# Optimization experiments

Hardware: AMD Instinct MI355X
Metric: run time of the kernel (lower is better)

Reference implementation:

```python
import jax, jax.numpy as jnp
import numpy as np

N_NODES = 100000
N_EDGES = 1600000
IN_DIM = 128
OUT_DIM = 10
N_GRAPHS = 512


def setup_inputs() -> dict:
    key = jax.random.key(0)
    ks = jax.random.split(key, 16)
    x = jax.random.normal(ks[0], (N_NODES, IN_DIM), dtype=jnp.float32)
    edge_index = jax.random.randint(ks[1], (2, N_EDGES), 0, N_NODES, dtype=jnp.int64)
    batch = jnp.sort(jax.random.randint(ks[2], (N_NODES,), 0, N_GRAPHS, dtype=jnp.int64))
    s = 0.1
    params = {
        'W1': jax.random.normal(ks[3], (IN_DIM, 32), dtype=jnp.float32) * s,
        'b1': jnp.zeros((32,), dtype=jnp.float32),
        'W2': jax.random.normal(ks[4], (32, 64), dtype=jnp.float32) * s,
        'b2': jnp.zeros((64,), dtype=jnp.float32),
        'W3': jax.random.normal(ks[5], (64, 128), dtype=jnp.float32) * s,
        'b3': jnp.zeros((128,), dtype=jnp.float32),
        'Wl1': jax.random.normal(ks[6], (128, 64), dtype=jnp.float32) * s,
        'bl1': jnp.zeros((64,), dtype=jnp.float32),
        'Wl2': jax.random.normal(ks[7], (64, OUT_DIM), dtype=jnp.float32) * s,
        'bl2': jnp.zeros((OUT_DIM,), dtype=jnp.float32),
    }
    return {'x': x, 'edge_index': edge_index, 'batch': batch, **params}


def _gcn_conv(x, src, dst, norm, W, b, n):
    # PyG GCNConv: out[i] = sum_j norm_ij * (x[j] @ W) + b, with self-loops folded into (src, dst).
    xw = x @ W                                   # [N, F_out]
    msg = xw[src] * norm[:, None]                # gather + scale  [E+N, F_out]
    return jax.ops.segment_sum(msg, dst, num_segments=n) + b


def reference(x, edge_index, batch, W1, b1, W2, b2, W3, b3, Wl1, bl1, Wl2, bl2):
    n = x.shape[0]
    loops = jnp.arange(n, dtype=edge_index.dtype)
    src = jnp.concatenate([edge_index[0], loops])  # j (source)
    dst = jnp.concatenate([edge_index[1], loops])  # i (target)
    # symmetric normalization D^{-1/2} (A+I) D^{-1/2}; degree at targets incl. self-loops
    deg = jax.ops.segment_sum(jnp.ones_like(dst, dtype=x.dtype), dst, num_segments=n)
    dinv = jnp.where(deg > 0, jax.lax.rsqrt(deg), 0.0)
    norm = dinv[src] * dinv[dst]
    # eval mode: dropout is identity
    h = jax.nn.relu(_gcn_conv(x, src, dst, norm, W1, b1, n))
    h = jax.nn.relu(_gcn_conv(h, src, dst, norm, W2, b2, n))
    h = _gcn_conv(h, src, dst, norm, W3, b3, n)
    g = jax.ops.segment_sum(h, batch, num_segments=N_GRAPHS)  # global_add_pool
    g = jax.nn.relu(g @ Wl1 + bl1)
    g = g @ Wl2 + bl2
    return jax.nn.log_softmax(g, axis=1)
```

## Files before the change

kernel.cpp:

```cpp
#include <hip/hip_runtime.h>
#include <hip/hip_bf16.h>
#include <math.h>
#include <type_traits>

#define NN 100000
#define NE 1600000
#define NG 512
#define NPB 128
#define NBUCK ((NN + NPB - 1) / NPB)
#define BCAP 3072
#define PBLOCKS 256
#define PTHREADS 1024

__device__ __forceinline__ float b2f(ushort u){ return __uint_as_float(((unsigned int)u)<<16); }
__device__ __forceinline__ ushort f2b(float f){
    __hip_bfloat16 h = __float2bfloat16(f);
    return *(ushort*)&h;
}
__device__ __forceinline__ float blo(unsigned int u){ return __uint_as_float(u<<16); }
__device__ __forceinline__ float bhi(unsigned int u){ return __uint_as_float(u & 0xffff0000u); }
__device__ __forceinline__ void acc4(float* a, uint2 u){
    a[0] += blo(u.x); a[1] += bhi(u.x); a[2] += blo(u.y); a[3] += bhi(u.y);
}
__device__ __forceinline__ void acc8(float* a, uint4 u){
    a[0] += blo(u.x); a[1] += bhi(u.x); a[2] += blo(u.y); a[3] += bhi(u.y);
    a[4] += blo(u.z); a[5] += bhi(u.z); a[6] += blo(u.w); a[7] += bhi(u.w);
}

__global__ __launch_bounds__(PTHREADS) void part_kernel(const int* __restrict__ src, const int* __restrict__ dst,
                                                        int* __restrict__ bucket_cnt, int* __restrict__ recs, int e){
    __shared__ int hist[NBUCK];
    __shared__ int base_[NBUCK];
    int tid = threadIdx.x;
    for(int b=tid; b<NBUCK; b+=PTHREADS) hist[b]=0;
    __syncthreads();
    int per = (e + PBLOCKS - 1) / PBLOCKS;
    per = (per + 3) & ~3;
    int lo = blockIdx.x * per;
    int hi = lo + per; if(hi > e) hi = e;
    if(lo >= hi) return;
    const int4* __restrict__ dst4 = (const int4*)dst;
    const int4* __restrict__ src4 = (const int4*)src;
    for(int i=lo/4+tid; i<hi/4; i+=PTHREADS){
        int4 d = dst4[i];
        atomicAdd(&hist[d.x>>7], 1);
        atomicAdd(&hist[d.y>>7], 1);
        atomicAdd(&hist[d.z>>7], 1);
        atomicAdd(&hist[d.w>>7], 1);
    }
    __syncthreads();
    for(int b=tid; b<NBUCK; b+=PTHREADS){
        int h = hist[b];
        base_[b] = h ? atomicAdd(&bucket_cnt[b], h) : 0;
        hist[b] = 0;
    }
    __syncthreads();
    for(int i=lo/4+tid; i<hi/4; i+=PTHREADS){
        int4 d = dst4[i];
        int4 s = src4[i];
        int b0=d.x>>7, b1=d.y>>7, b2=d.z>>7, b3=d.w>>7;
        int p0 = base_[b0] + atomicAdd(&hist[b0],1);
        int p1 = base_[b1] + atomicAdd(&hist[b1],1);
        int p2 = base_[b2] + atomicAdd(&hist[b2],1);
        int p3 = base_[b3] + atomicAdd(&hist[b3],1);
        if(p0 < BCAP) recs[(size_t)b0*BCAP + p0] = ((d.x & 127) << 17) | s.x;
        if(p1 < BCAP) recs[(size_t)b1*BCAP + p1] = ((d.y & 127) << 17) | s.y;
        if(p2 < BCAP) recs[(size_t)b2*BCAP + p2] = ((d.z & 127) << 17) | s.z;
        if(p3 < BCAP) recs[(size_t)b3*BCAP + p3] = ((d.w & 127) << 17) | s.w;
    }
}

__global__ __launch_bounds__(1024) void bucket_csr_kernel(const int* __restrict__ recs, const int* __restrict__ bucket_cnt,
                                                          int* __restrict__ csr, int* __restrict__ row_start,
                                                          int* __restrict__ row_end, float* __restrict__ dinv, int n){
    __shared__ int sr[BCAP];
    __shared__ int h[NPB];
    __shared__ int pc[NPB];
    __shared__ int cur[NPB];
    int b = blockIdx.x, tid = threadIdx.x;
    int cnt = bucket_cnt[b]; if(cnt > BCAP) cnt = BCAP;
    for(int i=tid; i<cnt; i+=1024) sr[i] = recs[(size_t)b*BCAP + i];
    if(tid < NPB) h[tid] = 0;
    __syncthreads();
    for(int i=tid; i<cnt; i+=1024) atomicAdd(&h[sr[i]>>17], 1);
    __syncthreads();
    int hp = (tid < NPB) ? ((h[tid]+3)&~3) : 0;
    if(tid < NPB) pc[tid] = hp;
    __syncthreads();
    for(int off=1; off<NPB; off<<=1){
        int t = (tid>=off && tid<NPB) ? pc[tid-off] : 0;
        __syncthreads();
        if(tid<NPB) pc[tid] += t;
        __syncthreads();
    }
    if(tid < NPB){
        int excl = pc[tid] - hp;
        cur[tid] = excl;
        int node = b*NPB + tid;
        if(node < n){
            row_start[node] = b*BCAP + excl;
            row_end[node]   = b*BCAP + excl + h[tid];
            dinv[node] = rsqrtf((float)(h[tid] + 1));
        }
    }
    __syncthreads();
    for(int i=tid; i<cnt; i+=1024){
        int rec = sr[i];
        int p = atomicAdd(&cur[rec>>17], 1);
        csr[(size_t)b*BCAP + p] = rec & 131071;
    }
}

template<int K, int NCOL, int RPT, bool BIAS, bool RELU, bool SCALE, bool BF16IN, bool BF16OUT>
__global__ __launch_bounds__(256) void gemm_kernel(const void* __restrict__ X_, const float* __restrict__ W,
                                                   const float* __restrict__ bias, const float* __restrict__ dinv,
                                                   void* __restrict__ Y_, int n){
    using TX = typename std::conditional<BF16IN, ushort, float>::type;
    const TX* __restrict__ X = (const TX*)X_;
    constexpr int CG = NCOL/4;
    constexpr int RT = 256/CG;
    constexpr int ROWS = RT*RPT;
    __shared__ float sW[K*NCOL];
    for(int i=threadIdx.x; i<K*NCOL/4; i+=256)
        ((float4*)sW)[i] = ((const float4*)W)[i];
    __syncthreads();
    int cg = threadIdx.x % CG;
    int rt = threadIdx.x / CG;
    int base = blockIdx.x*ROWS + rt*RPT;
    float acc[RPT][4];
    #pragma unroll
    for(int j=0;j<RPT;j++){ acc[j][0]=0.f; acc[j][1]=0.f; acc[j][2]=0.f; acc[j][3]=0.f; }
    const TX* xp[RPT];
    #pragma unroll
    for(int j=0;j<RPT;j++){
        int r = base+j; if(r>n-1) r=n-1;
        xp[j] = X + (size_t)r*K;
    }
    for(int k4=0;k4<K/4;k4++){
        float4 w0 = *(const float4*)&sW[(k4*4+0)*NCOL + cg*4];
        float4 w1 = *(const float4*)&sW[(k4*4+1)*NCOL + cg*4];
        float4 w2 = *(const float4*)&sW[(k4*4+2)*NCOL + cg*4];
        float4 w3 = *(const float4*)&sW[(k4*4+3)*NCOL + cg*4];
        #pragma unroll
        for(int j=0;j<RPT;j++){
            float4 xv;
            if constexpr(BF16IN){
                ushort4 xu = ((const ushort4*)xp[j])[k4];
                xv = make_float4(b2f(xu.x), b2f(xu.y), b2f(xu.z), b2f(xu.w));
            } else {
                xv = ((const float4*)xp[j])[k4];
            }
            acc[j][0] += xv.x*w0.x + xv.y*w1.x + xv.z*w2.x + xv.w*w3.x;
            acc[j][1] += xv.x*w0.y + xv.y*w1.y + xv.z*w2.y + xv.w*w3.y;
            acc[j][2] += xv.x*w0.z + xv.y*w1.z + xv.z*w2.z + xv.w*w3.z;
            acc[j][3] += xv.x*w0.w + xv.y*w1.w + xv.z*w2.w + xv.w*w3.w;
        }
    }
    float4 bv = make_float4(0.f,0.f,0.f,0.f);
    if constexpr(BIAS) bv = *(const float4*)&bias[cg*4];
    #pragma unroll
    for(int j=0;j<RPT;j++){
        int r = base+j;
        if(r<n){
            float4 o;
            o.x = acc[j][0]+bv.x; o.y = acc[j][1]+bv.y;
            o.z = acc[j][2]+bv.z; o.w = acc[j][3]+bv.w;
            if constexpr(RELU){
                o.x=fmaxf(o.x,0.f); o.y=fmaxf(o.y,0.f);
                o.z=fmaxf(o.z,0.f); o.w=fmaxf(o.w,0.f);
            }
            if constexpr(SCALE){
                float s = dinv[r];
                o.x*=s; o.y*=s; o.z*=s; o.w*=s;
            }
            if constexpr(BF16OUT){
                ushort4 u = make_ushort4(f2b(o.x), f2b(o.y), f2b(o.z), f2b(o.w));
                *(ushort4*)&((ushort*)Y_)[(size_t)r*NCOL + cg*4] = u;
            } else {
                *(float4*)&((float*)Y_)[(size_t)r*NCOL + cg*4] = o;
            }
        }
    }
}

template<int F, bool BIAS, bool RELU, bool POSTSCALE>
__global__ __launch_bounds__(256) void prop_kernel(const ushort* __restrict__ xin, ushort* __restrict__ xout,
                                                   const int* __restrict__ csr, const int* __restrict__ row_start,
                                                   const int* __restrict__ row_end, const float* __restrict__ dinv,
                                                   const float* __restrict__ bias, int n){
    constexpr int L = F/8;
    int gt  = blockIdx.x*256 + threadIdx.x;
    int node = gt / L;
    int f4   = gt & (L-1);
    if(node>=n) return;
    float di = dinv[node];
    const uint4* __restrict__ xw = ((const uint4*)xin) + f4;
    float a[8] = {0.f,0.f,0.f,0.f,0.f,0.f,0.f,0.f};
    float b[8] = {0.f,0.f,0.f,0.f,0.f,0.f,0.f,0.f};
    acc8(a, xw[(size_t)node*L]);
    int e  = row_start[node];
    int ee = row_end[node];
    for(; e+7<ee; e+=8){
        int4 c0 = *(const int4*)&csr[e];
        int4 c1 = *(const int4*)&csr[e+4];
        uint4 u0 = xw[(size_t)c0.x*L];
        uint4 u1 = xw[(size_t)c0.y*L];
        uint4 u2 = xw[(size_t)c0.z*L];
        uint4 u3 = xw[(size_t)c0.w*L];
        uint4 u4 = xw[(size_t)c1.x*L];
        uint4 u5 = xw[(size_t)c1.y*L];
        uint4 u6 = xw[(size_t)c1.z*L];
        uint4 u7 = xw[(size_t)c1.w*L];
        acc8(a,u0); acc8(b,u1); acc8(a,u2); acc8(b,u3);
        acc8(a,u4); acc8(b,u5); acc8(a,u6); acc8(b,u7);
    }
    if(e+3<ee){
        int4 c0 = *(const int4*)&csr[e];
        uint4 u0 = xw[(size_t)c0.x*L];
        uint4 u1 = xw[(size_t)c0.y*L];
        uint4 u2 = xw[(size_t)c0.z*L];
        uint4 u3 = xw[(size_t)c0.w*L];
        acc8(a,u0); acc8(b,u1); acc8(a,u2); acc8(b,u3);
        e += 4;
    }
    for(; e<ee; ++e) acc8(a, xw[(size_t)csr[e]*L]);
    float r[8];
    #pragma unroll
    for(int j=0;j<8;j++){
        r[j] = di*(a[j]+b[j]);
        if constexpr(BIAS) r[j] += bias[8*f4+j];
        if constexpr(RELU) r[j] = fmaxf(r[j],0.f);
        if constexpr(POSTSCALE) r[j] *= di;
    }
    uint4 outu;
    outu.x = ((unsigned int)f2b(r[1])<<16) | (unsigned int)f2b(r[0]);
    outu.y = ((unsigned int)f2b(r[3])<<16) | (unsigned int)f2b(r[2]);
    outu.z = ((unsigned int)f2b(r[5])<<16) | (unsigned int)f2b(r[4]);
    outu.w = ((unsigned int)f2b(r[7])<<16) | (unsigned int)f2b(r[6]);
    ((uint4*)xout)[(size_t)node*L + f4] = outu;
}

__global__ __launch_bounds__(256) void prop_gemm_kernel(const ushort* __restrict__ xin, ushort* __restrict__ xout,
                                                        const int* __restrict__ csr, const int* __restrict__ row_start,
                                                        const int* __restrict__ row_end, const float* __restrict__ dinv,
                                                        const float* __restrict__ W2, const float* __restrict__ b2, int n){
    __shared__ float4 sW2v[32*16];
    for(int i=threadIdx.x; i<512; i+=256) sW2v[i] = ((const float4*)W2)[i];
    __syncthreads();
    int gt  = blockIdx.x*256 + threadIdx.x;
    int node = gt >> 3;
    int og   = gt & 7;
    if(node >= n) return;
    float di = dinv[node];
    const uint2* __restrict__ xw = ((const uint2*)xin) + og;
    float a[4] = {0.f,0.f,0.f,0.f};
    float b[4] = {0.f,0.f,0.f,0.f};
    acc4(a, xw[(size_t)node*8]);
    int e  = row_start[node];
    int ee = row_end[node];
    for(; e+7<ee; e+=8){
        int4 c0 = *(const int4*)&csr[e];
        int4 c1 = *(const int4*)&csr[e+4];
        uint2 u0 = xw[(size_t)c0.x*8];
        uint2 u1 = xw[(size_t)c0.y*8];
        uint2 u2 = xw[(size_t)c0.z*8];
        uint2 u3 = xw[(size_t)c0.w*8];
        uint2 u4 = xw[(size_t)c1.x*8];
        uint2 u5 = xw[(size_t)c1.y*8];
        uint2 u6 = xw[(size_t)c1.z*8];
        uint2 u7 = xw[(size_t)c1.w*8];
        acc4(a,u0); acc4(b,u1); acc4(a,u2); acc4(b,u3);
        acc4(a,u4); acc4(b,u5); acc4(a,u6); acc4(b,u7);
    }
    if(e+3<ee){
        int4 c0 = *(const int4*)&csr[e];
        uint2 u0 = xw[(size_t)c0.x*8];
        uint2 u1 = xw[(size_t)c0.y*8];
        uint2 u2 = xw[(size_t)c0.z*8];
        uint2 u3 = xw[(size_t)c0.w*8];
        acc4(a,u0); acc4(b,u1); acc4(a,u2); acc4(b,u3);
        e += 4;
    }
    for(; e<ee; ++e) acc4(a, xw[(size_t)csr[e]*8]);
    float r[4];
    r[0] = di*(a[0]+b[0]);
    r[1] = di*(a[1]+b[1]);
    r[2] = di*(a[2]+b[2]);
    r[3] = di*(a[3]+b[3]);
    float acc[8] = {0.f,0.f,0.f,0.f,0.f,0.f,0.f,0.f};
    #pragma unroll
    for(int k=0;k<32;k++){
        float s = __shfl(r[k&3], k>>2, 8);
        float4 wa = sW2v[k*16 + og*2];
        float4 wb = sW2v[k*16 + og*2 + 1];
        acc[0]+=s*wa.x; acc[1]+=s*wa.y; acc[2]+=s*wa.z; acc[3]+=s*wa.w;
        acc[4]+=s*wb.x; acc[5]+=s*wb.y; acc[6]+=s*wb.z; acc[7]+=s*wb.w;
    }
    float4 ba = *(const float4*)&b2[og*8];
    float4 bb = *(const float4*)&b2[og*8+4];
    float o0 = di*fmaxf(acc[0]+ba.x, 0.f);
    float o1 = di*fmaxf(acc[1]+ba.y, 0.f);
    float o2 = di*fmaxf(acc[2]+ba.z, 0.f);
    float o3 = di*fmaxf(acc[3]+ba.w, 0.f);
    float o4 = di*fmaxf(acc[4]+bb.x, 0.f);
    float o5 = di*fmaxf(acc[5]+bb.y, 0.f);
    float o6 = di*fmaxf(acc[6]+bb.z, 0.f);
    float o7 = di*fmaxf(acc[7]+bb.w, 0.f);
    uint4 u;
    u.x = ((unsigned int)f2b(o1)<<16) | (unsigned int)f2b(o0);
    u.y = ((unsigned int)f2b(o3)<<16) | (unsigned int)f2b(o2);
    u.z = ((unsigned int)f2b(o5)<<16) | (unsigned int)f2b(o4);
    u.w = ((unsigned int)f2b(o7)<<16) | (unsigned int)f2b(o6);
    ((uint4*)xout)[(size_t)node*8 + og] = u;
}

__global__ __launch_bounds__(256) void prop_pool_kernel(const ushort* __restrict__ xin,
                                                        const int* __restrict__ csr, const int* __restrict__ row_start,
                                                        const int* __restrict__ row_end, const float* __restrict__ dinv,
                                                        const int* __restrict__ batch, float* __restrict__ pool, int n){
    __shared__ float sp[32*64];
    __shared__ int sg[32];
    int base = blockIdx.x*32;
    int tid = threadIdx.x;
    int node = base + (tid >> 3);
    int f4 = tid & 7;
    if(tid < 32) sg[tid] = batch[base+tid];
    float di = dinv[node];
    const uint4* __restrict__ xw = ((const uint4*)xin) + f4;
    float a[8] = {0.f,0.f,0.f,0.f,0.f,0.f,0.f,0.f};
    float b[8] = {0.f,0.f,0.f,0.f,0.f,0.f,0.f,0.f};
    acc8(a, xw[(size_t)node*8]);
    int e  = row_start[node];
    int ee = row_end[node];
    for(; e+7<ee; e+=8){
        int4 c0 = *(const int4*)&csr[e];
        int4 c1 = *(const int4*)&csr[e+4];
        uint4 u0 = xw[(size_t)c0.x*8];
        uint4 u1 = xw[(size_t)c0.y*8];
        uint4 u2 = xw[(size_t)c0.z*8];
        uint4 u3 = xw[(size_t)c0.w*8];
        uint4 u4 = xw[(size_t)c1.x*8];
        uint4 u5 = xw[(size_t)c1.y*8];
        uint4 u6 = xw[(size_t)c1.z*8];
        uint4 u7 = xw[(size_t)c1.w*8];
        acc8(a,u0); acc8(b,u1); acc8(a,u2); acc8(b,u3);
        acc8(a,u4); acc8(b,u5); acc8(a,u6); acc8(b,u7);
    }
    if(e+3<ee){
        int4 c0 = *(const int4*)&csr[e];
        uint4 u0 = xw[(size_t)c0.x*8];
        uint4 u1 = xw[(size_t)c0.y*8];
        uint4 u2 = xw[(size_t)c0.z*8];
        uint4 u3 = xw[(size_t)c0.w*8];
        acc8(a,u0); acc8(b,u1); acc8(a,u2); acc8(b,u3);
        e += 4;
    }
    for(; e<ee; ++e) acc8(a, xw[(size_t)csr[e]*8]);
    float4 r0, r1;
    r0.x = di*(a[0]+b[0]); r0.y = di*(a[1]+b[1]); r0.z = di*(a[2]+b[2]); r0.w = di*(a[3]+b[3]);
    r1.x = di*(a[4]+b[4]); r1.y = di*(a[5]+b[5]); r1.z = di*(a[6]+b[6]); r1.w = di*(a[7]+b[7]);
    ((float4*)sp)[tid*2]   = r0;
    ((float4*)sp)[tid*2+1] = r1;
    __syncthreads();
    if(tid < 64){
        int g0 = sg[0], g1 = sg[31];
        for(int g=g0; g<=g1; ++g){
            float s = 0.f;
            #pragma unroll
            for(int nl=0; nl<32; ++nl)
                if(sg[nl]==g) s += sp[nl*64 + tid];
            atomicAdd(&pool[g*64 + tid], s);
        }
    }
}

__global__ __launch_bounds__(128) void head_kernel(const float* __restrict__ pool, const int* __restrict__ batch, int n,
                                                   const float* __restrict__ W3, const float* __restrict__ b3,
                                                   const float* __restrict__ Wl1, const float* __restrict__ bl1,
                                                   const float* __restrict__ Wl2, const float* __restrict__ bl2,
                                                   float* __restrict__ out){
    __shared__ float sp[64];
    __shared__ float sg3[128];
    __shared__ float sh[64];
    __shared__ float sl[10];
    int g = blockIdx.x, t = threadIdx.x;
    if(t<64) sp[t] = pool[g*64+t];
    __syncthreads();
    int lo=0, hi=n;
    while(lo<hi){ int mid=(lo+hi)>>1; if(batch[mid]<g) lo=mid+1; else hi=mid; }
    int start=lo;
    lo=start; hi=n;
    while(lo<hi){ int mid=(lo+hi)>>1; if(batch[mid]<g+1) lo=mid+1; else hi=mid; }
    float cf = (float)(lo - start);
    float a = cf*b3[t];
    #pragma unroll 8
    for(int k=0;k<64;k++) a += sp[k]*W3[k*128+t];
    sg3[t]=a; __syncthreads();
    if(t<64){
        float h = bl1[t];
        #pragma unroll 8
        for(int k=0;k<128;k++) h += sg3[k]*Wl1[k*64+t];
        sh[t] = fmaxf(h,0.f);
    }
    __syncthreads();
    if(t<10){
        float l = bl2[t];
        for(int k=0;k<64;k++) l += sh[k]*Wl2[k*10+t];
        sl[t]=l;
    }
    __syncthreads();
    if(t<10){
        float m=sl[0];
        for(int k=1;k<10;k++) m=fmaxf(m,sl[k]);
        float s=0.f;
        for(int k=0;k<10;k++) s+=expf(sl[k]-m);
        out[g*10+t] = sl[t]-m-logf(s);
    }
}

extern "C" void kernel_launch(void* const* d_in, const int* in_sizes, int n_in,
                              void* d_out, int out_size, void* d_ws, size_t ws_size,
                              hipStream_t stream){
    const float* x   = (const float*)d_in[0];
    const int*   ei  = (const int*)d_in[1];
    const int* batch = (const int*)d_in[2];
    const float* W1  = (const float*)d_in[3];
    const float* b1  = (const float*)d_in[4];
    const float* W2  = (const float*)d_in[5];
    const float* b2  = (const float*)d_in[6];
    const float* W3  = (const float*)d_in[7];
    const float* b3  = (const float*)d_in[8];
    const float* Wl1 = (const float*)d_in[9];
    const float* bl1 = (const float*)d_in[10];
    const float* Wl2 = (const float*)d_in[11];
    const float* bl2 = (const float*)d_in[12];
    const int n = NN, E = NE;
    const int* src = ei;
    const int* dst = ei + E;

    char* ws = (char*)d_ws;
    size_t off = 0;
    auto alloc = [&](size_t bytes)->char*{
        char* p = ws + off;
        off = (off + bytes + 255) & ~(size_t)255;
        return p;
    };
    int*    bucket_cnt = (int*)   alloc((size_t)NBUCK*4);
    float*  dinv       = (float*) alloc((size_t)n*4);
    int*    recs       = (int*)   alloc((size_t)NBUCK*BCAP*4);
    int*    csr        = (int*)   alloc((size_t)NBUCK*BCAP*4);
    int*    row_start  = (int*)   alloc((size_t)n*4);
    int*    row_end    = (int*)   alloc((size_t)n*4);
    ushort* y1         = (ushort*)alloc((size_t)n*32*2);
    ushort* h1y        = (ushort*)alloc((size_t)n*32*2);
    ushort* h2y        = (ushort*)alloc((size_t)n*64*2);
    float*  pool       = (float*) alloc((size_t)NG*64*4);

    hipMemsetAsync(bucket_cnt, 0, (size_t)NBUCK*4, stream);
    hipMemsetAsync(pool, 0, (size_t)NG*64*4, stream);
    part_kernel<<<PBLOCKS,PTHREADS,0,stream>>>(src, dst, bucket_cnt, recs, E);
    bucket_csr_kernel<<<NBUCK,1024,0,stream>>>(recs, bucket_cnt, csr, row_start, row_end, dinv, n);

    gemm_kernel<128,32,2,false,false,true,false,true><<<(n+63)/64,256,0,stream>>>(x, W1, nullptr, dinv, y1, n);
    prop_kernel<32,true,true,true><<<(n*4+255)/256,256,0,stream>>>(y1, h1y, csr, row_start, row_end, dinv, b1, n);
    prop_gemm_kernel<<<(n*8+255)/256,256,0,stream>>>(h1y, h2y, csr, row_start, row_end, dinv, W2, b2, n);
    prop_pool_kernel<<<(n+31)/32,256,0,stream>>>(h2y, csr, row_start, row_end, dinv, batch, pool, n);
    head_kernel<<<NG,128,0,stream>>>(pool, batch, n, W3, b3, Wl1, bl1, Wl2, bl2, (float*)d_out);
}
```

Baseline: 259.9 us.

## Sort CSR neighbors by source range and merge the two workspace memsets

The bucket CSR build now keeps a histogram per (destination row, source sub-range of 16K nodes). Within each row, edges are placed in order of source range, so later gather-based propagation reads source features in a more local pattern. The scheme also spreads the shared-memory atomics over 8x more counters. The bucket-count and pool buffers are placed next to each other so a single memset clears both, removing one API call. The cost is a slightly larger histogram and serial 8-wide prefix loops in the CSR kernel.

```diff
diff --git a/kernel.cpp b/kernel.cpp
--- a/kernel.cpp
+++ b/kernel.cpp
@@ -74,18 +74,26 @@
                                                           int* __restrict__ csr, int* __restrict__ row_start,
                                                           int* __restrict__ row_end, float* __restrict__ dinv, int n){
     __shared__ int sr[BCAP];
-    __shared__ int h[NPB];
+    __shared__ int h2[NPB*8];
     __shared__ int pc[NPB];
-    __shared__ int cur[NPB];
+    __shared__ int hh[NPB];
     int b = blockIdx.x, tid = threadIdx.x;
     int cnt = bucket_cnt[b]; if(cnt > BCAP) cnt = BCAP;
     for(int i=tid; i<cnt; i+=1024) sr[i] = recs[(size_t)b*BCAP + i];
-    if(tid < NPB) h[tid] = 0;
-    __syncthreads();
-    for(int i=tid; i<cnt; i+=1024) atomicAdd(&h[sr[i]>>17], 1);
-    __syncthreads();
-    int hp = (tid < NPB) ? ((h[tid]+3)&~3) : 0;
-    if(tid < NPB) pc[tid] = hp;
+    h2[tid] = 0;
+    __syncthreads();
+    for(int i=tid; i<cnt; i+=1024){
+        int rec = sr[i];
+        atomicAdd(&h2[((rec>>17)<<3) | ((rec & 131071)>>14)], 1);
+    }
+    __syncthreads();
+    if(tid < NPB){
+        int s = 0;
+        #pragma unroll
+        for(int k=0;k<8;k++) s += h2[tid*8+k];
+        hh[tid] = s;
+        pc[tid] = (s+3)&~3;
+    }
     __syncthreads();
     for(int off=1; off<NPB; off<<=1){
         int t = (tid>=off && tid<NPB) ? pc[tid-off] : 0;
@@ -94,20 +102,24 @@
         __syncthreads();
     }
     if(tid < NPB){
+        int hp = (hh[tid]+3)&~3;
         int excl = pc[tid] - hp;
-        cur[tid] = excl;
+        int run = excl;
+        #pragma unroll
+        for(int k=0;k<8;k++){ int c = h2[tid*8+k]; h2[tid*8+k] = run; run += c; }
         int node = b*NPB + tid;
         if(node < n){
             row_start[node] = b*BCAP + excl;
-            row_end[node]   = b*BCAP + excl + h[tid];
-            dinv[node] = rsqrtf((float)(h[tid] + 1));
+            row_end[node]   = b*BCAP + excl + hh[tid];
+            dinv[node] = rsqrtf((float)(hh[tid] + 1));
         }
     }
     __syncthreads();
     for(int i=tid; i<cnt; i+=1024){
         int rec = sr[i];
-        int p = atomicAdd(&cur[rec>>17], 1);
-        csr[(size_t)b*BCAP + p] = rec & 131071;
+        int src = rec & 131071;
+        int p = atomicAdd(&h2[((rec>>17)<<3) | (src>>14)], 1);
+        csr[(size_t)b*BCAP + p] = src;
     }
 }
 
@@ -446,6 +458,8 @@
         return p;
     };
     int*    bucket_cnt = (int*)   alloc((size_t)NBUCK*4);
+    float*  pool       = (float*) alloc((size_t)NG*64*4);
+    size_t  zero_bytes = (size_t)((char*)pool - (char*)bucket_cnt) + (size_t)NG*64*4;
     float*  dinv       = (float*) alloc((size_t)n*4);
     int*    recs       = (int*)   alloc((size_t)NBUCK*BCAP*4);
     int*    csr        = (int*)   alloc((size_t)NBUCK*BCAP*4);
@@ -454,10 +468,8 @@
     ushort* y1         = (ushort*)alloc((size_t)n*32*2);
     ushort* h1y        = (ushort*)alloc((size_t)n*32*2);
     ushort* h2y        = (ushort*)alloc((size_t)n*64*2);
-    float*  pool       = (float*) alloc((size_t)NG*64*4);
-
-    hipMemsetAsync(bucket_cnt, 0, (size_t)NBUCK*4, stream);
-    hipMemsetAsync(pool, 0, (size_t)NG*64*4, stream);
+
+    hipMemsetAsync(bucket_cnt, 0, zero_bytes, stream);
     part_kernel<<<PBLOCKS,PTHREADS,0,stream>>>(src, dst, bucket_cnt, recs, E);
     bucket_csr_kernel<<<NBUCK,1024,0,stream>>>(recs, bucket_cnt, csr, row_start, row_end, dinv, n);
 
```

Measured after the change: 255.4 us. No clear change (-1.7%).
